# Kernel optimization log

Measured on AMD Instinct MI355X. Metric: run time of the kernel, lower is better.

## Reference

```python
import jax, jax.numpy as jnp
import numpy as np

PC = 512      # proposal_channels == conv_channels
INCH = 512    # in_channels of branch
B = 8
T = 64        # pyramid level length (feat_t) at order=0
TF = 256      # frame_level_feature length (clip_length)
KERNELS = [8, 16, 8, 4, 2, 2, 2]  # ConPoolingKernal
CLC = 498     # feature_lastclass channels (CLC + 2 == 500)
GROUPS = 32


def _gn(x, gamma, beta):
    # GroupNorm(32, C) over [B, C, L]
    Bb, C, L = x.shape
    xg = x.reshape(Bb, GROUPS, C // GROUPS, L)
    m = xg.mean(axis=(2, 3), keepdims=True)
    v = xg.var(axis=(2, 3), keepdims=True)
    xn = ((xg - m) * jax.lax.rsqrt(v + 1e-5)).reshape(Bb, C, L)
    return xn * gamma[None, :, None] + beta[None, :, None]


def _c1(x, w, b):
    # Unit1D kernel_shape=1: pointwise conv
    return jnp.einsum('bct,oc->bot', x, w) + b[None, :, None]


def _bmp(feat, segs):
    # BoundaryMaxPooling: first C/2 channels max-pooled over segs[...,0:2],
    # second C/2 over segs[...,2:4] (inclusive integer ranges, clamped).
    Bb, C, L = feat.shape
    C2 = C // 2
    pos = jnp.arange(L)
    def pool(f, s, e):
        s = jnp.clip(s, 0, L - 1)
        e = jnp.maximum(jnp.clip(e, 0, L - 1), s)
        mask = (pos[None, None, :] >= s[..., None]) & (pos[None, None, :] <= e[..., None])  # [B,T,L]
        return jnp.max(jnp.where(mask[:, None], f[:, :, None, :], -jnp.inf), axis=-1)  # [B,C2,T]
    return jnp.concatenate([pool(feat[:, :C2], segs[..., 0], segs[..., 1]),
                            pool(feat[:, C2:], segs[..., 2], segs[..., 3])], axis=1)


def _anchor_gather(feat, anc, K):
    # Vectorized per-anchor clamp/slice + nearest F.interpolate(size=K):
    # src index for output k of a slice [l, r] is l + floor(k * (r - l + 1) / K).
    Bb, C, L = feat.shape
    left = jnp.clip(anc[..., 0], 0, L)
    right = jnp.clip(anc[..., 1], 0, L)
    valid = right > left                      # empty slices -> zeros (torch branch)
    seglen = right + 1 - left
    k = jnp.arange(K)
    idx = jnp.clip(left[..., None] + (k[None, None, :] * seglen[..., None]) // K, 0, L - 1)  # [B,T,K]
    g = jax.vmap(lambda f, ix: f[:, ix])(feat, idx)   # [B,C,T,K]
    return g * valid[:, None, :, None].astype(feat.dtype)


def setup_inputs() -> dict:
    key = jax.random.key(0)
    ks = jax.random.split(key, 16)
    f32 = jnp.float32
    s = 0.02
    def w(k, shape):
        return jax.random.normal(k, shape, f32) * s
    inp = {}
    inp['feature'] = jax.random.normal(ks[0], (B, INCH, T), f32)
    inp['frame_level_feature'] = jax.random.normal(ks[1], (B, PC, TF), f32)
    inp['segments'] = jax.random.randint(ks[2], (B, T, 4), 0, T).astype(jnp.int32)
    inp['frame_segments'] = jax.random.randint(ks[3], (B, T, 4), 0, TF).astype(jnp.int32)
    inp['feature_lastclass'] = jax.random.normal(ks[4], (B, CLC, T), f32)
    inp['anchor'] = jnp.sort(jax.random.randint(ks[5], (B, T, 2), 0, T), axis=-1).astype(jnp.int32)
    inp['frame_anchor'] = jnp.sort(jax.random.randint(ks[6], (B, T, 2), 0, TF), axis=-1).astype(jnp.int32)
    inp['order'] = 0
    inp['LocResult_feature'] = jax.random.normal(ks[7], (B, 2, T), f32)
    inp['w_cur'] = w(ks[8], (PC, INCH)); inp['b_cur'] = jnp.zeros((PC,), f32)
    inp['g_cur'] = jnp.ones((PC,), f32); inp['be_cur'] = jnp.zeros((PC,), f32)
    inp['w_lr'] = w(ks[9], (2 * PC, INCH)); inp['b_lr'] = jnp.zeros((2 * PC,), f32)
    inp['g_lr'] = jnp.ones((2 * PC,), f32); inp['be_lr'] = jnp.zeros((2 * PC,), f32)
    inp['w_roi'] = w(ks[10], (PC, PC)); inp['b_roi'] = jnp.zeros((PC,), f32)
    inp['g_roi'] = jnp.ones((PC,), f32); inp['be_roi'] = jnp.zeros((PC,), f32)
    K1 = KERNELS[1]; K0 = KERNELS[0]
    inp['w_cp'] = w(ks[11], (PC, 2 * PC, K1)); inp['b_cp'] = jnp.zeros((PC,), f32)
    inp['w_cp0'] = w(ks[12], (PC, PC, K0)); inp['b_cp0'] = jnp.zeros((PC,), f32)
    CIN = 6 * PC + 500
    inp['w_prop'] = w(ks[13], (INCH, CIN)); inp['b_prop'] = jnp.zeros((INCH,), f32)
    inp['g_prop'] = jnp.ones((INCH,), f32); inp['be_prop'] = jnp.zeros((INCH,), f32)
    return inp


def reference(feature, frame_level_feature, segments, frame_segments, feature_lastclass,
              anchor, frame_anchor, order, LocResult_feature,
              w_cur, b_cur, g_cur, be_cur, w_lr, b_lr, g_lr, be_lr,
              w_roi, b_roi, g_roi, be_roi, w_cp, b_cp, w_cp0, b_cp0,
              w_prop, b_prop, g_prop, be_prop):
    relu = jax.nn.relu
    fm_short = relu(_gn(_c1(feature, w_cur, b_cur), g_cur, be_cur))           # [B,PC,T]
    feat_lr = relu(_gn(_c1(feature, w_lr, b_lr), g_lr, be_lr))                # [B,2PC,T]
    prop_feature = _bmp(feat_lr, segments)                                    # [B,2PC,T]
    prop_roi = relu(_gn(_c1(_bmp(frame_level_feature, frame_segments), w_roi, b_roi), g_roi, be_roi))
    K1 = KERNELS[order + 1]
    K0 = KERNELS[0]
    g1 = _anchor_gather(feat_lr, anchor, K1)                                  # [B,2PC,T,K1]
    con_feature = jnp.einsum('bctk,ock->bot', g1, w_cp) + b_cp[None, :, None]  # valid conv K1->1
    g0 = _anchor_gather(frame_level_feature, frame_anchor, K0)                # [B,PC,T,K0]
    frame_con = jnp.einsum('bctk,ock->bot', g0, w_cp0) + b_cp0[None, :, None]
    prop_con = relu(_gn(_c1(frame_con, w_roi, b_roi), g_roi, be_roi))
    cat = jnp.concatenate([prop_roi, prop_feature, fm_short, feature_lastclass,
                           con_feature, prop_con, LocResult_feature], axis=1)  # [B,6PC+500,T]
    out = relu(_gn(_c1(cat, w_prop, b_prop), g_prop, be_prop))                # [B,INCH,T]
    return (out, feat_lr)
```

## Files before the change

kernel.cpp:

```cpp
#include <hip/hip_runtime.h>
#include <math.h>

#define BB 8
#define CATP 3584
#define CAT_REAL 3572

typedef __attribute__((ext_vector_type(8))) short short8;
typedef __attribute__((ext_vector_type(4))) float f32x4;

__device__ inline ushort f2bf(float f) {
  union { float f; unsigned u; } x;
  x.f = f;
  return (ushort)((x.u + 0x7FFFu + ((x.u >> 16) & 1u)) >> 16);
}
__device__ inline float bf2f(unsigned us) {
  union { unsigned u; float f; } x;
  x.u = us << 16;
  return x.f;
}

template <int Cin, int Kf>
__device__ void cpT_tile(const float* __restrict__ W, ushort* __restrict__ D,
                         int nt, int cc) {
  const int tid = threadIdx.x;
  const int j = tid >> 6, l4 = (tid >> 4) & 3, l15 = tid & 15;
  const int o = nt * 64 + j * 16 + l15;
  const int cb = cc * 32 + l4 * 8;
  ushort rg[8][Kf];
#pragma unroll
  for (int q = 0; q < 8; q++) {
    const float* row = W + ((size_t)o * Cin + cb + q) * Kf;
#pragma unroll
    for (int kq = 0; kq < Kf / 4; kq++) {
      const float4 f = *(const float4*)(row + kq * 4);
      rg[q][kq * 4 + 0] = f2bf(f.x);
      rg[q][kq * 4 + 1] = f2bf(f.y);
      rg[q][kq * 4 + 2] = f2bf(f.z);
      rg[q][kq * 4 + 3] = f2bf(f.w);
    }
  }
#pragma unroll
  for (int k = 0; k < Kf; k++) {
    uint4 pk;
    pk.x = (unsigned)rg[0][k] | ((unsigned)rg[1][k] << 16);
    pk.y = (unsigned)rg[2][k] | ((unsigned)rg[3][k] << 16);
    pk.z = (unsigned)rg[4][k] | ((unsigned)rg[5][k] << 16);
    pk.w = (unsigned)rg[6][k] | ((unsigned)rg[7][k] << 16);
    *(uint4*)(D + ((size_t)(nt * Kf + k) * (Cin >> 5) + cc) * 2048 + tid * 8) = pk;
  }
}

__global__ __launch_bounds__(256) void prep_kernel(
    const float* __restrict__ w_cur, const float* __restrict__ w_lr,
    const float* __restrict__ w_roi, const float* __restrict__ w_prop,
    ushort* __restrict__ Wcomb, ushort* __restrict__ Wroi,
    ushort* __restrict__ Wprop, const float* __restrict__ w_cp,
    ushort* __restrict__ WcpT, const float* __restrict__ w_cp0,
    ushort* __restrict__ Wcp0T, const float* __restrict__ feature,
    const float* __restrict__ frame_feat, const float* __restrict__ lastcls,
    const float* __restrict__ locres, ushort* __restrict__ Ft,
    ushort* __restrict__ FfT, ushort* __restrict__ cat) {
  __shared__ float tile[64 * 65];
  const int bid = blockIdx.x;
  if (bid < 1408) {
    const int i = bid * 256 + threadIdx.x;
    const float* src;
    ushort* dst;
    int o, k8, Kc;
    bool pad = false;
    if (i < 98304) {
      o = i >> 6; k8 = i & 63; Kc = 16;
      src = (o < 512) ? (w_cur + (size_t)o * 512)
                      : (w_lr + (size_t)(o - 512) * 512);
      dst = Wcomb;
    } else if (i < 131072) {
      const int r = i - 98304;
      o = r >> 6; k8 = r & 63; Kc = 16;
      src = w_roi + (size_t)o * 512;
      dst = Wroi;
    } else {
      const int r = i - 131072;
      if (r >= 229376) return;
      o = r / 448; k8 = r % 448; Kc = 112;
      src = w_prop + (size_t)o * CAT_REAL;
      dst = Wprop;
      pad = true;
    }
    const int k = k8 * 8;
    float v[8];
    if (pad) {
#pragma unroll
      for (int q = 0; q < 8; q++) v[q] = (k + q < CAT_REAL) ? src[k + q] : 0.f;
    } else {
      const float4 f0 = *(const float4*)(src + k);
      const float4 f1 = *(const float4*)(src + k + 4);
      v[0] = f0.x; v[1] = f0.y; v[2] = f0.z; v[3] = f0.w;
      v[4] = f1.x; v[5] = f1.y; v[6] = f1.z; v[7] = f1.w;
    }
    uint4 pk;
    pk.x = (unsigned)f2bf(v[0]) | ((unsigned)f2bf(v[1]) << 16);
    pk.y = (unsigned)f2bf(v[2]) | ((unsigned)f2bf(v[3]) << 16);
    pk.z = (unsigned)f2bf(v[4]) | ((unsigned)f2bf(v[5]) << 16);
    pk.w = (unsigned)f2bf(v[6]) | ((unsigned)f2bf(v[7]) << 16);
    const int ot = o >> 6, ii = (o >> 4) & 3, l15 = o & 15;
    const int kc = k8 >> 2, l4 = k8 & 3;
    const size_t flat =
        ((((size_t)ot * Kc + kc) * 4 + ii) * 64 + l4 * 16 + l15) * 8;
    *(uint4*)(dst + flat) = pk;
    return;
  }
  if (bid < 1792) {
    const int local = bid - 1408;
    if (local < 256)
      cpT_tile<1024, 16>(w_cp, WcpT, local >> 5, local & 31);
    else {
      const int r = local - 256;
      cpT_tile<512, 8>(w_cp0, Wcp0T, r >> 4, r & 15);
    }
    return;
  }
  const int local = bid - 1792;
  const float* src;
  ushort* dst;
  int Cr, Cw, L, rs, co, cblk, lblk, b;
  if (local < 64) {
    src = feature; dst = Ft; Cr = 512; Cw = 512; L = 64; rs = 512; co = 0;
    cblk = local & 7; lblk = 0; b = local >> 3;
  } else if (local < 320) {
    const int r = local - 64;
    src = frame_feat; dst = FfT; Cr = 512; Cw = 512; L = 256; rs = 512; co = 0;
    cblk = r & 7; lblk = (r >> 3) & 3; b = r >> 5;
  } else if (local < 384) {
    const int r = local - 320;
    src = lastcls; dst = cat; Cr = 498; Cw = 498; L = 64; rs = CATP; co = 2048;
    cblk = r & 7; lblk = 0; b = r >> 3;
  } else {
    const int r = local - 384;
    src = locres; dst = cat; Cr = 2; Cw = 14; L = 64; rs = CATP; co = 3570;
    cblk = 0; lblk = 0; b = r;
  }
  const int c0 = cblk * 64, l0 = lblk * 64;
  for (int e = threadIdx.x; e < 4096; e += 256) {
    const int cc = e >> 6, ll = e & 63;
    const int c = c0 + cc;
    tile[cc * 65 + ll] = (c < Cr) ? src[((size_t)b * Cr + c) * L + l0 + ll] : 0.f;
  }
  __syncthreads();
  for (int e = threadIdx.x; e < 4096; e += 256) {
    const int ll = e >> 6, cc = e & 63;
    const int c = c0 + cc;
    if (c < Cw)
      dst[((size_t)b * L + l0 + ll) * rs + co + c] = f2bf(tile[cc * 65 + ll]);
  }
}

__device__ void gemm_gn_body(const ushort* __restrict__ Xt,
                             const ushort* __restrict__ Wb,
                             const float* __restrict__ bias,
                             const float* __restrict__ gamma,
                             const float* __restrict__ beta, int Kp,
                             int cpgShift, float* __restrict__ outF, int outFM,
                             ushort* __restrict__ catOut, int catStride,
                             int chOff, int ot, int b, float* smem) {
  float* red = smem;
  float* rs = smem + 4224;
  float* rss = smem + 4228;
  float* gmean = smem + 4232;
  float* grstd = smem + 4236;
  const int w = threadIdx.x >> 6;
  const int lane = threadIdx.x & 63;
  const int l15 = lane & 15, l4 = lane >> 4;
  const int o0 = ot * 64;

  f32x4 acc[4] = {};
  const ushort* wbase = Wb + (size_t)ot * (Kp >> 5) * 2048 + lane * 8;
  const ushort* bp[4];
#pragma unroll
  for (int j = 0; j < 4; j++)
    bp[j] = Xt + (size_t)(b * 64 + j * 16 + l15) * Kp + l4 * 8;
  const int nkc = Kp >> 5;
  for (int kc = 0; kc < nkc; kc++) {
    const short8 a = *(const short8*)(wbase + ((size_t)kc * 4 + w) * 512);
    short8 x[4];
#pragma unroll
    for (int j = 0; j < 4; j++) x[j] = *(const short8*)(bp[j] + kc * 32);
#pragma unroll
    for (int j = 0; j < 4; j++)
      acc[j] = __builtin_amdgcn_mfma_f32_16x16x32_bf16(a, x[j], acc[j], 0, 0, 0);
  }
#pragma unroll
  for (int j = 0; j < 4; j++)
#pragma unroll
    for (int r = 0; r < 4; r++) {
      const int m = w * 16 + l4 * 4 + r;
      red[m * 65 + j * 16 + l15] = acc[j][r] + bias[o0 + m];
    }
  __syncthreads();

  const int cpg = 1 << cpgShift;
  const int ngroups = 64 >> cpgShift;
  for (int gi = 0; gi < ngroups; gi++) {
    float s = 0.f, ss = 0.f;
    const int nel = cpg << 6;
    for (int e = threadIdx.x; e < nel; e += 256) {
      const float v = red[((gi << cpgShift) + (e >> 6)) * 65 + (e & 63)];
      s += v;
      ss += v * v;
    }
#pragma unroll
    for (int off = 32; off > 0; off >>= 1) {
      s += __shfl_down(s, off);
      ss += __shfl_down(ss, off);
    }
    if (lane == 0) { rs[w] = s; rss[w] = ss; }
    __syncthreads();
    if (threadIdx.x == 0) {
      const float ts = rs[0] + rs[1] + rs[2] + rs[3];
      const float tss = rss[0] + rss[1] + rss[2] + rss[3];
      const float mean = ts / (float)nel;
      const float var = tss / (float)nel - mean * mean;
      gmean[gi] = mean;
      grstd[gi] = rsqrtf(var + 1e-5f);
    }
    __syncthreads();
  }

  if (outF) {
    for (int e = threadIdx.x; e < 4096; e += 256) {
      const int m = e >> 6, n = e & 63;
      const int gi = m >> cpgShift;
      const int c = o0 + m;
      float v = (red[m * 65 + n] - gmean[gi]) * grstd[gi] * gamma[c] + beta[c];
      v = fmaxf(v, 0.f);
      outF[((size_t)b * outFM + c) * 64 + n] = v;
    }
  }
  if (catOut) {
    for (int e = threadIdx.x; e < 4096; e += 256) {
      const int n = e >> 6, m = e & 63;
      const int gi = m >> cpgShift;
      const int c = o0 + m;
      float v = (red[m * 65 + n] - gmean[gi]) * grstd[gi] * gamma[c] + beta[c];
      v = fmaxf(v, 0.f);
      catOut[((size_t)(b * 64) + n) * catStride + chOff + c] = f2bf(v);
    }
  }
}

__device__ void gemm_part_body(const ushort* __restrict__ Xt,
                               const ushort* __restrict__ Wb,
                               float* __restrict__ P, int ot, int b, int slice,
                               int kbeg, int kend) {
  const int w = threadIdx.x >> 6;
  const int lane = threadIdx.x & 63;
  const int l15 = lane & 15, l4 = lane >> 4;
  f32x4 acc[4] = {};
  const ushort* wbase = Wb + (size_t)ot * (CATP >> 5) * 2048 + lane * 8;
  const ushort* bp[4];
#pragma unroll
  for (int j = 0; j < 4; j++)
    bp[j] = Xt + (size_t)(b * 64 + j * 16 + l15) * CATP + l4 * 8;
  for (int k = kbeg; k < kend; k += 32) {
    const int kc = k >> 5;
    const short8 a = *(const short8*)(wbase + ((size_t)kc * 4 + w) * 512);
    short8 x[4];
#pragma unroll
    for (int j = 0; j < 4; j++) x[j] = *(const short8*)(bp[j] + k);
#pragma unroll
    for (int j = 0; j < 4; j++)
      acc[j] = __builtin_amdgcn_mfma_f32_16x16x32_bf16(a, x[j], acc[j], 0, 0, 0);
  }
  float* Pp = P + (((size_t)slice * BB + b) * 512 + ot * 64) * 64;
#pragma unroll
  for (int j = 0; j < 4; j++)
#pragma unroll
    for (int r = 0; r < 4; r++)
      Pp[(w * 16 + l4 * 4 + r) * 64 + j * 16 + l15] = acc[j][r];
}

__global__ __launch_bounds__(256) void reduce_gn_kernel(
    const ushort* __restrict__ cat, const ushort* __restrict__ Wprop,
    const float* __restrict__ P, const float* __restrict__ bias,
    const float* __restrict__ gamma, const float* __restrict__ beta,
    float* __restrict__ outF) {
  const int ot = blockIdx.x;
  const int b = blockIdx.y;
  const int o0 = ot * 64;
  const int w = threadIdx.x >> 6;
  const int lane = threadIdx.x & 63;
  const int l15 = lane & 15, l4 = lane >> 4;

  f32x4 acc[4] = {};
  const ushort* wbase = Wprop + (size_t)ot * (CATP >> 5) * 2048 + lane * 8;
  const ushort* bp[4];
#pragma unroll
  for (int j = 0; j < 4; j++)
    bp[j] = cat + (size_t)(b * 64 + j * 16 + l15) * CATP + l4 * 8;
  for (int k = 2528; k < 3584; k += 32) {
    const int kc = k >> 5;
    const short8 a = *(const short8*)(wbase + ((size_t)kc * 4 + w) * 512);
    short8 x[4];
#pragma unroll
    for (int j = 0; j < 4; j++) x[j] = *(const short8*)(bp[j] + k);
#pragma unroll
    for (int j = 0; j < 4; j++)
      acc[j] = __builtin_amdgcn_mfma_f32_16x16x32_bf16(a, x[j], acc[j], 0, 0, 0);
  }

  __shared__ float red[64 * 65];
#pragma unroll
  for (int j = 0; j < 4; j++)
#pragma unroll
    for (int r = 0; r < 4; r++)
      red[(w * 16 + l4 * 4 + r) * 65 + j * 16 + l15] = acc[j][r];
  __syncthreads();
  for (int e = threadIdx.x; e < 4096; e += 256) {
    const int m = e >> 6, n = e & 63;
    float s = bias[o0 + m];
#pragma unroll
    for (int z = 0; z < 4; z++)
      s += P[(((size_t)z * BB + b) * 512 + o0 + m) * 64 + n];
    red[m * 65 + n] += s;
  }
  __syncthreads();
  __shared__ float rs[4], rss[4], gmean[4], grstd[4];
  for (int gi = 0; gi < 4; gi++) {
    float s = 0.f, ss = 0.f;
    for (int e = threadIdx.x; e < 1024; e += 256) {
      const float v = red[((gi << 4) + (e >> 6)) * 65 + (e & 63)];
      s += v;
      ss += v * v;
    }
#pragma unroll
    for (int off = 32; off > 0; off >>= 1) {
      s += __shfl_down(s, off);
      ss += __shfl_down(ss, off);
    }
    if (lane == 0) { rs[w] = s; rss[w] = ss; }
    __syncthreads();
    if (threadIdx.x == 0) {
      const float ts = rs[0] + rs[1] + rs[2] + rs[3];
      const float tss = rss[0] + rss[1] + rss[2] + rss[3];
      const float mean = ts / 1024.f;
      const float var = tss / 1024.f - mean * mean;
      gmean[gi] = mean;
      grstd[gi] = rsqrtf(var + 1e-5f);
    }
    __syncthreads();
  }
  for (int e = threadIdx.x; e < 4096; e += 256) {
    const int m = e >> 6, n = e & 63;
    const int gi = m >> 4;
    const int c = o0 + m;
    float v = (red[m * 65 + n] - gmean[gi]) * grstd[gi] * gamma[c] + beta[c];
    outF[((size_t)b * 512 + c) * 64 + n] = fmaxf(v, 0.f);
  }
}

template <int C, int L>
__device__ void bmp_body(const ushort* __restrict__ Xt,
                         const int* __restrict__ segs, ushort* __restrict__ Y,
                         int rowStride, int chOff, int t, int b,
                         float2 (*pmax)[512]) {
  constexpr int C2 = C / 2;
  constexpr int P2 = C2 / 2;
  constexpr int CH = P2 / 64;
  const int w = threadIdx.x >> 6;
  const int lane = threadIdx.x & 63;
  const int* sg = segs + ((size_t)b * 64 + t) * 4;
  const ushort* Xb = Xt + (size_t)b * L * C;
#pragma unroll
  for (int h = 0; h < 2; h++) {
    const int s = min(max(sg[2 * h], 0), L - 1);
    const int e = max(min(max(sg[2 * h + 1], 0), L - 1), s);
#pragma unroll
    for (int q = 0; q < CH; q++) {
      const int p = q * 64 + lane;
      const ushort* base = Xb + h * C2 + 2 * p;
      float a0 = -INFINITY, a1 = -INFINITY;
      float c0 = -INFINITY, c1 = -INFINITY;
      int l = s + w;
      for (; l + 4 <= e; l += 8) {
        const unsigned u0 = *(const unsigned*)(base + (size_t)l * C);
        const unsigned u1 = *(const unsigned*)(base + (size_t)(l + 4) * C);
        a0 = fmaxf(a0, bf2f(u0 & 0xffffu));
        a1 = fmaxf(a1, bf2f(u0 >> 16));
        c0 = fmaxf(c0, bf2f(u1 & 0xffffu));
        c1 = fmaxf(c1, bf2f(u1 >> 16));
      }
      if (l <= e) {
        const unsigned u0 = *(const unsigned*)(base + (size_t)l * C);
        a0 = fmaxf(a0, bf2f(u0 & 0xffffu));
        a1 = fmaxf(a1, bf2f(u0 >> 16));
      }
      pmax[w][h * P2 + p] = make_float2(fmaxf(a0, c0), fmaxf(a1, c1));
    }
  }
  __syncthreads();
  for (int idx = threadIdx.x; idx < 2 * P2; idx += 256) {
    float2 m = pmax[0][idx];
#pragma unroll
    for (int ww = 1; ww < 4; ww++) {
      const float2 v = pmax[ww][idx];
      m.x = fmaxf(m.x, v.x);
      m.y = fmaxf(m.y, v.y);
    }
    const unsigned o = (unsigned)f2bf(m.x) | ((unsigned)f2bf(m.y) << 16);
    *(unsigned*)(Y + ((size_t)(b * 64) + t) * rowStride + chOff + 2 * idx) = o;
  }
}

template <int Kf, int L, int Cin, int NT, int CSPAN>
__device__ void anchor_body2(const ushort* __restrict__ src,
                             const int* __restrict__ anc,
                             const ushort* __restrict__ Wt,
                             float* __restrict__ P, int nt, int b, int tapbase,
                             int cbase, int slice) {
  const int w = threadIdx.x >> 6;
  const int lane = threadIdx.x & 63;
  const int l15 = lane & 15, l4 = lane >> 4;
  const int t = w * 16 + l15;
  const int a0 = anc[((size_t)b * 64 + t) * 2 + 0];
  const int a1 = anc[((size_t)b * 64 + t) * 2 + 1];
  const int left = min(max(a0, 0), L);
  const int right = min(max(a1, 0), L);
  const int seglen = right + 1 - left;

  f32x4 acc[4] = {};
#pragma unroll
  for (int kt = 0; kt < NT; kt++) {
    const int k = tapbase + kt;
    const int ix = min(max(left + (k * seglen) / Kf, 0), L - 1);
    const ushort* rp = src + ((size_t)b * L + ix) * Cin + cbase + l4 * 8;
    const ushort* wb = Wt + ((size_t)nt * Kf + k) * (Cin >> 5) * 2048 + lane * 8;
#pragma unroll 4
    for (int c0 = 0; c0 < CSPAN; c0 += 32) {
      const int cc = (cbase + c0) >> 5;
      const short8 a = *(const short8*)(rp + c0);
      short8 bbf[4];
#pragma unroll
      for (int j = 0; j < 4; j++)
        bbf[j] = *(const short8*)(wb + ((size_t)cc * 4 + j) * 512);
#pragma unroll
      for (int j = 0; j < 4; j++)
        acc[j] =
            __builtin_amdgcn_mfma_f32_16x16x32_bf16(a, bbf[j], acc[j], 0, 0, 0);
    }
  }
  float* Pp = P + (((size_t)slice * BB + b) * 64) * 512 + nt * 64;
#pragma unroll
  for (int j = 0; j < 4; j++)
#pragma unroll
    for (int r = 0; r < 4; r++)
      Pp[(size_t)(w * 16 + l4 * 4 + r) * 512 + j * 16 + l15] = acc[j][r];
}

__device__ void anchor_reduce_body(const float* __restrict__ P, int ks,
                                   const float* __restrict__ bias,
                                   const int* __restrict__ anc, int L,
                                   ushort* __restrict__ Y, int rowStride,
                                   int chOff, int ot, int b, float* smem) {
  float* tile = smem;
  float* sval = smem + 4160;
  const int o0 = ot * 64;
  if (threadIdx.x < 64) {
    const int t = threadIdx.x;
    const int a0 = anc[((size_t)b * 64 + t) * 2 + 0];
    const int a1 = anc[((size_t)b * 64 + t) * 2 + 1];
    const int left = min(max(a0, 0), L);
    const int right = min(max(a1, 0), L);
    sval[t] = (right > left) ? 1.f : 0.f;
  }
  __syncthreads();
  for (int e = threadIdx.x; e < 4096; e += 256) {
    const int m = e >> 6, nl = e & 63;
    float s = 0.f;
    for (int z = 0; z < ks; z++)
      s += P[(((size_t)z * BB + b) * 64 + m) * 512 + o0 + nl];
    tile[nl * 65 + m] = s * sval[m] + bias[o0 + nl];
  }
  __syncthreads();
  for (int e = threadIdx.x; e < 4096; e += 256) {
    const int m = e >> 6, nl = e & 63;
    Y[((size_t)(b * 64) + m) * rowStride + chOff + o0 + nl] =
        f2bf(tile[nl * 65 + m]);
  }
}

__global__ __launch_bounds__(256) void fused_B_kernel(
    const ushort* __restrict__ Ft, const ushort* __restrict__ Wcomb,
    const float* __restrict__ b_cur, const float* __restrict__ g_cur,
    const float* __restrict__ be_cur, ushort* __restrict__ cat,
    const float* __restrict__ b_lr, const float* __restrict__ g_lr,
    const float* __restrict__ be_lr, float* __restrict__ feat_lr,
    ushort* __restrict__ FlrT, const ushort* __restrict__ FfT,
    const int* __restrict__ frame_segs, ushort* __restrict__ XbmpT,
    const int* __restrict__ frame_anchor, const ushort* __restrict__ Wcp0T,
    float* __restrict__ P0) {
  __shared__ __align__(16) float smem[4240];
  const int bid = blockIdx.x;
  if (bid < 512) {
    const int nt = bid & 7, b = (bid >> 3) & 7, s = bid >> 6;
    anchor_body2<8, 256, 512, 1, 512>(FfT, frame_anchor, Wcp0T, P0, nt, b, s,
                                      0, s);
  } else if (bid < 704) {
    const int r = bid - 512;
    const int b = r / 24, ot24 = r % 24;
    if (ot24 < 8)
      gemm_gn_body(Ft, Wcomb, b_cur, g_cur, be_cur, 512, 4, nullptr, 0, cat,
                   CATP, 1536, ot24, b, smem);
    else
      gemm_gn_body(Ft, Wcomb + 512 * 512, b_lr, g_lr, be_lr, 512, 5, feat_lr,
                   1024, FlrT, 1024, 0, ot24 - 8, b, smem);
  } else {
    const int r = bid - 704;
    bmp_body<512, 256>(FfT, frame_segs, XbmpT, 512, 0, r & 63, r >> 6,
                       (float2(*)[512])smem);
  }
}

__global__ __launch_bounds__(256) void fused_C_kernel(
    const ushort* __restrict__ FlrT, const int* __restrict__ segments,
    ushort* __restrict__ cat, const int* __restrict__ anchor,
    const ushort* __restrict__ WcpT, float* __restrict__ P1,
    const float* __restrict__ P0, const float* __restrict__ b_cp0,
    const int* __restrict__ frame_anchor, ushort* __restrict__ FconT,
    const ushort* __restrict__ XbmpT, const ushort* __restrict__ Wroi,
    const float* __restrict__ b_roi, const float* __restrict__ g_roi,
    const float* __restrict__ be_roi) {
  __shared__ __align__(16) float smem[4240];
  const int bid = blockIdx.x;
  if (bid < 1024) {
    const int nt = bid & 7, b = (bid >> 3) & 7, s = bid >> 6;
    const int kz = s >> 1, ch = s & 1;
    anchor_body2<16, 64, 1024, 2, 512>(FlrT, anchor, WcpT, P1, nt, b, kz * 2,
                                       ch * 512, s);
  } else if (bid < 1088) {
    const int r = bid - 1024;
    gemm_gn_body(XbmpT, Wroi, b_roi, g_roi, be_roi, 512, 4, nullptr, 0, cat,
                 CATP, 0, r & 7, r >> 3, smem);
  } else if (bid < 1152) {
    const int r = bid - 1088;
    anchor_reduce_body(P0, 8, b_cp0, frame_anchor, 256, FconT, 512, 0, r & 7,
                       r >> 3, smem);
  } else {
    const int r = bid - 1152;
    bmp_body<1024, 64>(FlrT, segments, cat, CATP, 512, r & 63, r >> 6,
                       (float2(*)[512])smem);
  }
}

__global__ __launch_bounds__(256) void fused_D_kernel(
    const ushort* __restrict__ cat, const ushort* __restrict__ Wprop,
    float* __restrict__ P9, const float* __restrict__ P1,
    const float* __restrict__ b_cp, const int* __restrict__ anchor,
    ushort* __restrict__ catw, const ushort* __restrict__ FconT,
    const ushort* __restrict__ Wroi, const float* __restrict__ b_roi,
    const float* __restrict__ g_roi, const float* __restrict__ be_roi) {
  __shared__ __align__(16) float smem[4240];
  const int bid = blockIdx.x;
  if (bid < 256) {
    const int s = bid >> 6, q = bid & 63;
    const int kb = s * 640;
    const int ke = (s == 3) ? 2528 : kb + 640;
    gemm_part_body(cat, Wprop, P9, q & 7, q >> 3, s, kb, ke);
  } else if (bid < 320) {
    const int r = bid - 256;
    anchor_reduce_body(P1, 16, b_cp, anchor, 64, catw, CATP, 2546, r & 7,
                       r >> 3, smem);
  } else {
    const int r = bid - 320;
    gemm_gn_body(FconT, Wroi, b_roi, g_roi, be_roi, 512, 4, nullptr, 0, catw,
                 CATP, 3058, r & 7, r >> 3, smem);
  }
}

extern "C" void kernel_launch(void* const* d_in, const int* in_sizes, int n_in,
                              void* d_out, int out_size, void* d_ws,
                              size_t ws_size, hipStream_t stream) {
  const float* feature      = (const float*)d_in[0];
  const float* frame_feat   = (const float*)d_in[1];
  const int*   segments     = (const int*)d_in[2];
  const int*   frame_segs   = (const int*)d_in[3];
  const float* feat_lastcls = (const float*)d_in[4];
  const int*   anchor       = (const int*)d_in[5];
  const int*   frame_anchor = (const int*)d_in[6];
  const float* locres       = (const float*)d_in[8];
  const float* w_cur  = (const float*)d_in[9];
  const float* b_cur  = (const float*)d_in[10];
  const float* g_cur  = (const float*)d_in[11];
  const float* be_cur = (const float*)d_in[12];
  const float* w_lr   = (const float*)d_in[13];
  const float* b_lr   = (const float*)d_in[14];
  const float* g_lr   = (const float*)d_in[15];
  const float* be_lr  = (const float*)d_in[16];
  const float* w_roi  = (const float*)d_in[17];
  const float* b_roi  = (const float*)d_in[18];
  const float* g_roi  = (const float*)d_in[19];
  const float* be_roi = (const float*)d_in[20];
  const float* w_cp   = (const float*)d_in[21];
  const float* b_cp   = (const float*)d_in[22];
  const float* w_cp0  = (const float*)d_in[23];
  const float* b_cp0  = (const float*)d_in[24];
  const float* w_prop = (const float*)d_in[25];
  const float* b_prop = (const float*)d_in[26];
  const float* g_prop = (const float*)d_in[27];
  const float* be_prop= (const float*)d_in[28];

  float* out_main = (float*)d_out;
  float* feat_lr  = (float*)d_out + BB * 512 * 64;

  ushort* cat_t  = (ushort*)d_ws;
  ushort* Ft     = cat_t + 1835008;
  ushort* XbmpT  = Ft + 262144;
  ushort* FconT  = XbmpT + 262144;
  ushort* Wcomb  = FconT + 262144;
  ushort* Wroi   = Wcomb + 786432;
  ushort* Wprop  = Wroi + 262144;
  ushort* WcpT   = Wprop + 1835008;
  ushort* Wcp0T  = WcpT + 8388608;
  ushort* FlrT   = Wcp0T + 2097152;
  ushort* FfT    = FlrT + 524288;
  float*  P1     = (float*)(FfT + 1048576);
  float*  P0     = P1 + 4194304;
  float*  P9     = P0 + 2097152;

  prep_kernel<<<2184, 256, 0, stream>>>(
      w_cur, w_lr, w_roi, w_prop, Wcomb, Wroi, Wprop, w_cp, WcpT, w_cp0,
      Wcp0T, feature, frame_feat, feat_lastcls, locres, Ft, FfT, cat_t);

  fused_B_kernel<<<1216, 256, 0, stream>>>(
      Ft, Wcomb, b_cur, g_cur, be_cur, cat_t, b_lr, g_lr, be_lr, feat_lr,
      FlrT, FfT, frame_segs, XbmpT, frame_anchor, Wcp0T, P0);

  fused_C_kernel<<<1664, 256, 0, stream>>>(
      FlrT, segments, cat_t, anchor, WcpT, P1, P0, b_cp0, frame_anchor, FconT,
      XbmpT, Wroi, b_roi, g_roi, be_roi);

  fused_D_kernel<<<384, 256, 0, stream>>>(
      cat_t, Wprop, P9, P1, b_cp, anchor, cat_t, FconT, Wroi, b_roi, g_roi,
      be_roi);

  reduce_gn_kernel<<<dim3(8, BB), 256, 0, stream>>>(
      cat_t, Wprop, P9, b_prop, g_prop, be_prop, out_main);
}
```

Before: 298.2 us.

## Defer late weight conversions into fused_B and batch anchor GEMMs over four batches

The conversion of w_roi, w_prop and w_cp, which later stages need, moves out of the first prep kernel and into fused_B as extra blocks, so it overlaps with the early GEMM and pooling work. The anchor-gather GEMMs are rewritten so each block handles one tap across four batches. This reuses each loaded weight fragment for four batches and splits the work over more tap and channel slices. The partial buffers P0 and P1 double in size and the reduce kernels sum over twice as many slices, which adds memory traffic and register pressure.

```diff
diff --git a/kernel.cpp b/kernel.cpp
--- a/kernel.cpp
+++ b/kernel.cpp
@@ -17,6 +17,32 @@
   union { unsigned u; float f; } x;
   x.u = us << 16;
   return x.f;
+}
+
+__device__ inline void wfrag_conv(const float* __restrict__ srcrow,
+                                  ushort* __restrict__ dst, int o, int k8,
+                                  int Kc, int Kreal) {
+  const int k = k8 * 8;
+  float v[8];
+  if (Kreal > 0) {
+#pragma unroll
+    for (int q = 0; q < 8; q++) v[q] = (k + q < Kreal) ? srcrow[k + q] : 0.f;
+  } else {
+    const float4 f0 = *(const float4*)(srcrow + k);
+    const float4 f1 = *(const float4*)(srcrow + k + 4);
+    v[0] = f0.x; v[1] = f0.y; v[2] = f0.z; v[3] = f0.w;
+    v[4] = f1.x; v[5] = f1.y; v[6] = f1.z; v[7] = f1.w;
+  }
+  uint4 pk;
+  pk.x = (unsigned)f2bf(v[0]) | ((unsigned)f2bf(v[1]) << 16);
+  pk.y = (unsigned)f2bf(v[2]) | ((unsigned)f2bf(v[3]) << 16);
+  pk.z = (unsigned)f2bf(v[4]) | ((unsigned)f2bf(v[5]) << 16);
+  pk.w = (unsigned)f2bf(v[6]) | ((unsigned)f2bf(v[7]) << 16);
+  const int ot = o >> 6, ii = (o >> 4) & 3, l15 = o & 15;
+  const int kc = k8 >> 2, l4 = k8 & 3;
+  const size_t flat =
+      ((((size_t)ot * Kc + kc) * 4 + ii) * 64 + l4 * 16 + l15) * 8;
+  *(uint4*)(dst + flat) = pk;
 }
 
 template <int Cin, int Kf>
@@ -50,76 +76,29 @@
   }
 }
 
-__global__ __launch_bounds__(256) void prep_kernel(
+__global__ __launch_bounds__(256) void prep_early_kernel(
     const float* __restrict__ w_cur, const float* __restrict__ w_lr,
-    const float* __restrict__ w_roi, const float* __restrict__ w_prop,
-    ushort* __restrict__ Wcomb, ushort* __restrict__ Wroi,
-    ushort* __restrict__ Wprop, const float* __restrict__ w_cp,
-    ushort* __restrict__ WcpT, const float* __restrict__ w_cp0,
+    ushort* __restrict__ Wcomb, const float* __restrict__ w_cp0,
     ushort* __restrict__ Wcp0T, const float* __restrict__ feature,
     const float* __restrict__ frame_feat, const float* __restrict__ lastcls,
     const float* __restrict__ locres, ushort* __restrict__ Ft,
     ushort* __restrict__ FfT, ushort* __restrict__ cat) {
   __shared__ float tile[64 * 65];
   const int bid = blockIdx.x;
-  if (bid < 1408) {
+  if (bid < 384) {
     const int i = bid * 256 + threadIdx.x;
-    const float* src;
-    ushort* dst;
-    int o, k8, Kc;
-    bool pad = false;
-    if (i < 98304) {
-      o = i >> 6; k8 = i & 63; Kc = 16;
-      src = (o < 512) ? (w_cur + (size_t)o * 512)
-                      : (w_lr + (size_t)(o - 512) * 512);
-      dst = Wcomb;
-    } else if (i < 131072) {
-      const int r = i - 98304;
-      o = r >> 6; k8 = r & 63; Kc = 16;
-      src = w_roi + (size_t)o * 512;
-      dst = Wroi;
-    } else {
-      const int r = i - 131072;
-      if (r >= 229376) return;
-      o = r / 448; k8 = r % 448; Kc = 112;
-      src = w_prop + (size_t)o * CAT_REAL;
-      dst = Wprop;
-      pad = true;
-    }
-    const int k = k8 * 8;
-    float v[8];
-    if (pad) {
-#pragma unroll
-      for (int q = 0; q < 8; q++) v[q] = (k + q < CAT_REAL) ? src[k + q] : 0.f;
-    } else {
-      const float4 f0 = *(const float4*)(src + k);
-      const float4 f1 = *(const float4*)(src + k + 4);
-      v[0] = f0.x; v[1] = f0.y; v[2] = f0.z; v[3] = f0.w;
-      v[4] = f1.x; v[5] = f1.y; v[6] = f1.z; v[7] = f1.w;
-    }
-    uint4 pk;
-    pk.x = (unsigned)f2bf(v[0]) | ((unsigned)f2bf(v[1]) << 16);
-    pk.y = (unsigned)f2bf(v[2]) | ((unsigned)f2bf(v[3]) << 16);
-    pk.z = (unsigned)f2bf(v[4]) | ((unsigned)f2bf(v[5]) << 16);
-    pk.w = (unsigned)f2bf(v[6]) | ((unsigned)f2bf(v[7]) << 16);
-    const int ot = o >> 6, ii = (o >> 4) & 3, l15 = o & 15;
-    const int kc = k8 >> 2, l4 = k8 & 3;
-    const size_t flat =
-        ((((size_t)ot * Kc + kc) * 4 + ii) * 64 + l4 * 16 + l15) * 8;
-    *(uint4*)(dst + flat) = pk;
+    const int o = i >> 6, k8 = i & 63;
+    const float* srcrow = (o < 512) ? w_cur + (size_t)o * 512
+                                    : w_lr + (size_t)(o - 512) * 512;
+    wfrag_conv(srcrow, Wcomb, o, k8, 16, 0);
     return;
   }
-  if (bid < 1792) {
-    const int local = bid - 1408;
-    if (local < 256)
-      cpT_tile<1024, 16>(w_cp, WcpT, local >> 5, local & 31);
-    else {
-      const int r = local - 256;
-      cpT_tile<512, 8>(w_cp0, Wcp0T, r >> 4, r & 15);
-    }
+  if (bid < 512) {
+    const int r = bid - 384;
+    cpT_tile<512, 8>(w_cp0, Wcp0T, r >> 4, r & 15);
     return;
   }
-  const int local = bid - 1792;
+  const int local = bid - 512;
   const float* src;
   ushort* dst;
   int Cr, Cw, L, rs, co, cblk, lblk, b;
@@ -410,49 +389,58 @@
   }
 }
 
-template <int Kf, int L, int Cin, int NT, int CSPAN>
-__device__ void anchor_body2(const ushort* __restrict__ src,
+template <int Kf, int L, int Cin, int CSPAN, int BG>
+__device__ void anchor_body3(const ushort* __restrict__ src,
                              const int* __restrict__ anc,
                              const ushort* __restrict__ Wt,
-                             float* __restrict__ P, int nt, int b, int tapbase,
+                             float* __restrict__ P, int nt, int b0, int k,
                              int cbase, int slice) {
   const int w = threadIdx.x >> 6;
   const int lane = threadIdx.x & 63;
   const int l15 = lane & 15, l4 = lane >> 4;
   const int t = w * 16 + l15;
-  const int a0 = anc[((size_t)b * 64 + t) * 2 + 0];
-  const int a1 = anc[((size_t)b * 64 + t) * 2 + 1];
-  const int left = min(max(a0, 0), L);
-  const int right = min(max(a1, 0), L);
-  const int seglen = right + 1 - left;
-
-  f32x4 acc[4] = {};
-#pragma unroll
-  for (int kt = 0; kt < NT; kt++) {
-    const int k = tapbase + kt;
+
+  const ushort* rp[BG];
+#pragma unroll
+  for (int bi = 0; bi < BG; bi++) {
+    const int b = b0 + bi;
+    const int a0 = anc[((size_t)b * 64 + t) * 2 + 0];
+    const int a1 = anc[((size_t)b * 64 + t) * 2 + 1];
+    const int left = min(max(a0, 0), L);
+    const int right = min(max(a1, 0), L);
+    const int seglen = right + 1 - left;
     const int ix = min(max(left + (k * seglen) / Kf, 0), L - 1);
-    const ushort* rp = src + ((size_t)b * L + ix) * Cin + cbase + l4 * 8;
-    const ushort* wb = Wt + ((size_t)nt * Kf + k) * (Cin >> 5) * 2048 + lane * 8;
-#pragma unroll 4
-    for (int c0 = 0; c0 < CSPAN; c0 += 32) {
-      const int cc = (cbase + c0) >> 5;
-      const short8 a = *(const short8*)(rp + c0);
-      short8 bbf[4];
+    rp[bi] = src + ((size_t)b * L + ix) * Cin + cbase + l4 * 8;
+  }
+  const ushort* wb = Wt + ((size_t)nt * Kf + k) * (Cin >> 5) * 2048 + lane * 8;
+
+  f32x4 acc[BG][4] = {};
+#pragma unroll 2
+  for (int c0 = 0; c0 < CSPAN; c0 += 32) {
+    const int cc = (cbase + c0) >> 5;
+    short8 bbf[4];
+#pragma unroll
+    for (int j = 0; j < 4; j++)
+      bbf[j] = *(const short8*)(wb + ((size_t)cc * 4 + j) * 512);
+    short8 a[BG];
+#pragma unroll
+    for (int bi = 0; bi < BG; bi++) a[bi] = *(const short8*)(rp[bi] + c0);
+#pragma unroll
+    for (int bi = 0; bi < BG; bi++)
 #pragma unroll
       for (int j = 0; j < 4; j++)
-        bbf[j] = *(const short8*)(wb + ((size_t)cc * 4 + j) * 512);
-#pragma unroll
-      for (int j = 0; j < 4; j++)
-        acc[j] =
-            __builtin_amdgcn_mfma_f32_16x16x32_bf16(a, bbf[j], acc[j], 0, 0, 0);
-    }
-  }
-  float* Pp = P + (((size_t)slice * BB + b) * 64) * 512 + nt * 64;
-#pragma unroll
-  for (int j = 0; j < 4; j++)
-#pragma unroll
-    for (int r = 0; r < 4; r++)
-      Pp[(size_t)(w * 16 + l4 * 4 + r) * 512 + j * 16 + l15] = acc[j][r];
+        acc[bi][j] = __builtin_amdgcn_mfma_f32_16x16x32_bf16(a[bi], bbf[j],
+                                                             acc[bi][j], 0, 0, 0);
+  }
+#pragma unroll
+  for (int bi = 0; bi < BG; bi++) {
+    float* Pp = P + (((size_t)slice * BB + b0 + bi) * 64) * 512 + nt * 64;
+#pragma unroll
+    for (int j = 0; j < 4; j++)
+#pragma unroll
+      for (int r = 0; r < 4; r++)
+        Pp[(size_t)(w * 16 + l4 * 4 + r) * 512 + j * 16 + l15] = acc[bi][j][r];
+  }
 }
 
 __device__ void anchor_reduce_body(const float* __restrict__ P, int ks,
@@ -496,15 +484,18 @@
     ushort* __restrict__ FlrT, const ushort* __restrict__ FfT,
     const int* __restrict__ frame_segs, ushort* __restrict__ XbmpT,
     const int* __restrict__ frame_anchor, const ushort* __restrict__ Wcp0T,
-    float* __restrict__ P0) {
+    float* __restrict__ P0, const float* __restrict__ w_roi,
+    ushort* __restrict__ Wroi, const float* __restrict__ w_prop,
+    ushort* __restrict__ Wprop, const float* __restrict__ w_cp,
+    ushort* __restrict__ WcpT) {
   __shared__ __align__(16) float smem[4240];
   const int bid = blockIdx.x;
-  if (bid < 512) {
-    const int nt = bid & 7, b = (bid >> 3) & 7, s = bid >> 6;
-    anchor_body2<8, 256, 512, 1, 512>(FfT, frame_anchor, Wcp0T, P0, nt, b, s,
-                                      0, s);
-  } else if (bid < 704) {
-    const int r = bid - 512;
+  if (bid < 256) {
+    const int nt = bid & 7, bg = (bid >> 3) & 1, s = bid >> 4;
+    anchor_body3<8, 256, 512, 256, 4>(FfT, frame_anchor, Wcp0T, P0, nt,
+                                      bg * 4, s >> 1, (s & 1) * 256, s);
+  } else if (bid < 448) {
+    const int r = bid - 256;
     const int b = r / 24, ot24 = r % 24;
     if (ot24 < 8)
       gemm_gn_body(Ft, Wcomb, b_cur, g_cur, be_cur, 512, 4, nullptr, 0, cat,
@@ -512,10 +503,20 @@
     else
       gemm_gn_body(Ft, Wcomb + 512 * 512, b_lr, g_lr, be_lr, 512, 5, feat_lr,
                    1024, FlrT, 1024, 0, ot24 - 8, b, smem);
-  } else {
-    const int r = bid - 704;
+  } else if (bid < 960) {
+    const int r = bid - 448;
     bmp_body<512, 256>(FfT, frame_segs, XbmpT, 512, 0, r & 63, r >> 6,
                        (float2(*)[512])smem);
+  } else if (bid < 1088) {
+    const int r = (bid - 960) * 256 + threadIdx.x;
+    wfrag_conv(w_roi + (size_t)(r >> 6) * 512, Wroi, r >> 6, r & 63, 16, 0);
+  } else if (bid < 1984) {
+    const int r = (bid - 1088) * 256 + threadIdx.x;
+    wfrag_conv(w_prop + (size_t)(r / 448) * CAT_REAL, Wprop, r / 448, r % 448,
+               112, CAT_REAL);
+  } else {
+    const int local = bid - 1984;
+    cpT_tile<1024, 16>(w_cp, WcpT, local >> 5, local & 31);
   }
 }
 
@@ -530,21 +531,20 @@
     const float* __restrict__ be_roi) {
   __shared__ __align__(16) float smem[4240];
   const int bid = blockIdx.x;
-  if (bid < 1024) {
-    const int nt = bid & 7, b = (bid >> 3) & 7, s = bid >> 6;
-    const int kz = s >> 1, ch = s & 1;
-    anchor_body2<16, 64, 1024, 2, 512>(FlrT, anchor, WcpT, P1, nt, b, kz * 2,
-                                       ch * 512, s);
-  } else if (bid < 1088) {
-    const int r = bid - 1024;
+  if (bid < 512) {
+    const int nt = bid & 7, bg = (bid >> 3) & 1, s = bid >> 4;
+    anchor_body3<16, 64, 1024, 512, 4>(FlrT, anchor, WcpT, P1, nt, bg * 4,
+                                       s >> 1, (s & 1) * 512, s);
+  } else if (bid < 576) {
+    const int r = bid - 512;
     gemm_gn_body(XbmpT, Wroi, b_roi, g_roi, be_roi, 512, 4, nullptr, 0, cat,
                  CATP, 0, r & 7, r >> 3, smem);
-  } else if (bid < 1152) {
-    const int r = bid - 1088;
-    anchor_reduce_body(P0, 8, b_cp0, frame_anchor, 256, FconT, 512, 0, r & 7,
+  } else if (bid < 640) {
+    const int r = bid - 576;
+    anchor_reduce_body(P0, 16, b_cp0, frame_anchor, 256, FconT, 512, 0, r & 7,
                        r >> 3, smem);
   } else {
-    const int r = bid - 1152;
+    const int r = bid - 640;
     bmp_body<1024, 64>(FlrT, segments, cat, CATP, 512, r & 63, r >> 6,
                        (float2(*)[512])smem);
   }
@@ -566,7 +566,7 @@
     gemm_part_body(cat, Wprop, P9, q & 7, q >> 3, s, kb, ke);
   } else if (bid < 320) {
     const int r = bid - 256;
-    anchor_reduce_body(P1, 16, b_cp, anchor, 64, catw, CATP, 2546, r & 7,
+    anchor_reduce_body(P1, 32, b_cp, anchor, 64, catw, CATP, 2546, r & 7,
                        r >> 3, smem);
   } else {
     const int r = bid - 320;
@@ -622,18 +622,19 @@
   ushort* FlrT   = Wcp0T + 2097152;
   ushort* FfT    = FlrT + 524288;
   float*  P1     = (float*)(FfT + 1048576);
-  float*  P0     = P1 + 4194304;
-  float*  P9     = P0 + 2097152;
-
-  prep_kernel<<<2184, 256, 0, stream>>>(
-      w_cur, w_lr, w_roi, w_prop, Wcomb, Wroi, Wprop, w_cp, WcpT, w_cp0,
-      Wcp0T, feature, frame_feat, feat_lastcls, locres, Ft, FfT, cat_t);
-
-  fused_B_kernel<<<1216, 256, 0, stream>>>(
+  float*  P0     = P1 + 8388608;
+  float*  P9     = P0 + 4194304;
+
+  prep_early_kernel<<<904, 256, 0, stream>>>(
+      w_cur, w_lr, Wcomb, w_cp0, Wcp0T, feature, frame_feat, feat_lastcls,
+      locres, Ft, FfT, cat_t);
+
+  fused_B_kernel<<<2240, 256, 0, stream>>>(
       Ft, Wcomb, b_cur, g_cur, be_cur, cat_t, b_lr, g_lr, be_lr, feat_lr,
-      FlrT, FfT, frame_segs, XbmpT, frame_anchor, Wcp0T, P0);
-
-  fused_C_kernel<<<1664, 256, 0, stream>>>(
+      FlrT, FfT, frame_segs, XbmpT, frame_anchor, Wcp0T, P0, w_roi, Wroi,
+      w_prop, Wprop, w_cp, WcpT);
+
+  fused_C_kernel<<<1152, 256, 0, stream>>>(
       FlrT, segments, cat_t, anchor, WcpT, P1, P0, b_cp0, frame_anchor, FconT,
       XbmpT, Wroi, b_roi, g_roi, be_roi);
 
```

Result: slower. 349.9 us (+17.3%).
